# Kernel optimization log

Hardware: AMD Instinct MI355X
Metric: run time of the kernel (lower is better)

## Reference

```python
import jax, jax.numpy as jnp
import numpy as np

D = 512
N_WAY = 64
K_SHOT = 16
N_QUERY = 8192


def setup_inputs() -> dict:
    key = jax.random.key(0)
    k1, k2, k3, k4 = jax.random.split(key, 4)
    support = jax.random.normal(k1, (N_WAY * K_SHOT, D), dtype=jnp.float32)
    query = jax.random.normal(k2, (N_QUERY, D), dtype=jnp.float32)
    # nn.Linear(input_dim, input_dim) params (kaiming-uniform-ish scale)
    bound = 1.0 / np.sqrt(D)
    W = jax.random.uniform(k3, (D, D), minval=-bound, maxval=bound, dtype=jnp.float32)
    b = jax.random.uniform(k4, (D,), minval=-bound, maxval=bound, dtype=jnp.float32)
    return {"support": support, "query": query, "W": W, "b": b,
            "n_way": N_WAY, "k_shot": K_SHOT}


def reference(support, query, W, b, n_way, k_shot):
    # shared linear projection: x @ W^T + b (torch nn.Linear convention)
    support_emb = support @ W.T + b            # [n_way*k_shot, d]
    query_emb = query @ W.T + b                # [n_q, d]
    # class prototypes: mean over the k_shot axis
    prototypes = support_emb.reshape(n_way, k_shot, -1).mean(axis=1)  # [n_way, d]
    # pairwise squared euclidean distances (broadcast sub/square/sum,
    # same math as the torch euclidean_dist)
    diff = query_emb[:, None, :] - prototypes[None, :, :]  # [n_q, n_way, d]
    dists = jnp.sum(diff * diff, axis=-1)                  # [n_q, n_way]
    return dists
```

## Files before the change

### kernel.cpp

```cpp
#include <hip/hip_runtime.h>
#include <hip/hip_bf16.h>

#define D 512
#define NWAY 64
#define KSHOT 16
#define NQ 8192

typedef __bf16 bf16_t;
typedef __bf16 bf16x8_t __attribute__((ext_vector_type(8)));
typedef __bf16 bf16x4_t __attribute__((ext_vector_type(4)));
typedef float  f32x4    __attribute__((ext_vector_type(4)));

typedef __attribute__((address_space(1))) const void gv_t;
typedef __attribute__((address_space(3))) void lv_t;
__device__ __forceinline__ void ld16(const void* g, void* l) {
    __builtin_amdgcn_global_load_lds((gv_t*)g, (lv_t*)l, 16, 0, 0);
}


__global__ __launch_bounds__(256) void k_prep1(
    const float* __restrict__ sup, const float* __restrict__ W,
    const float* __restrict__ bias, float* __restrict__ Pg,
    bf16_t* __restrict__ Bsw)
{
    const int b = blockIdx.x, t = threadIdx.x;

    if (b < 256) {
        const int c = b >> 2, jq = b & 3;
        __shared__ __align__(16) float cm[D];
        {
            const int d = t * 2;
            float sx = 0.f, sy = 0.f;
#pragma unroll
            for (int j = 0; j < KSHOT; ++j) {
                float2 v = *(const float2*)(sup + (size_t)(c * KSHOT + j) * D + d);
                sx += v.x; sy += v.y;
            }
            cm[d] = sx * (1.0f / KSHOT); cm[d + 1] = sy * (1.0f / KSHOT);
        }
        __syncthreads();
        const int j = jq * 128 + (t >> 1);
        const int half = t & 1;
        const f32x4* wr = (const f32x4*)(W + (size_t)j * D + half * 256);
        const f32x4* cr = (const f32x4*)(cm + half * 256);
        float s = 0.f;
#pragma unroll 8
        for (int i = 0; i < 64; ++i) {
            f32x4 a = cr[i], wv = wr[i];
            s += a[0]*wv[0] + a[1]*wv[1] + a[2]*wv[2] + a[3]*wv[3];
        }
        s += __shfl_xor(s, 1);
        if (!half) Pg[(size_t)c * D + j] = s + bias[j];
        return;
    }

    {
        const int n = (b - 256) * 4 + (t >> 6);
        const int sl = t & 63;
        const f32x4* wp = (const f32x4*)(W + (size_t)n * D + sl * 8);
        f32x4 v0 = wp[0], v1 = wp[1];
        bf16x8_t hv = { (bf16_t)v0[0], (bf16_t)v0[1], (bf16_t)v0[2], (bf16_t)v0[3],
                        (bf16_t)v1[0], (bf16_t)v1[1], (bf16_t)v1[2], (bf16_t)v1[3] };
        const int ck = sl >> 3, s = sl & 7;
        *(bf16x8_t*)(Bsw + (size_t)ck * 36864 + n * 64 + ((s ^ (n & 7)) * 8)) = hv;
    }
}

__global__ __launch_bounds__(256) void k_prep2(
    const float* __restrict__ Pg, const float* __restrict__ W,
    const float* __restrict__ bias, bf16_t* __restrict__ Bsw,
    float* __restrict__ ph)
{
    __shared__ __align__(16) float Pl[D];
    __shared__ float sG[2][128];
    __shared__ float red[4];

    const int c = blockIdx.x >> 2, kc = blockIdx.x & 3;
    const int t = threadIdx.x;
    const int kl = t & 127, jh = t >> 7;
    const int k = kc * 128 + kl;

    ((float2*)Pl)[t] = ((const float2*)(Pg + (size_t)c * D))[t];
    __syncthreads();

    float g = 0.f;
    const float* wcol = W + (size_t)jh * 256 * D + k;
#pragma unroll 8
    for (int j = 0; j < 256; ++j)
        g += Pl[jh * 256 + j] * wcol[(size_t)j * D];
    sG[jh][kl] = g;

    if (kc == 0) {
        float v1 = Pl[t], v2 = Pl[t + 256];
        float pp = v1 * v1 - 2.0f * bias[t] * v1 + v2 * v2 - 2.0f * bias[t + 256] * v2;
#pragma unroll
        for (int off = 32; off; off >>= 1) pp += __shfl_xor(pp, off);
        if ((t & 63) == 0) red[t >> 6] = pp;
    }
    __syncthreads();

    if (jh == 0) {
        const float gt = sG[0][kl] + sG[1][kl];
        const int n = 512 + c;
        const int ck = k >> 6, s = (k >> 3) & 7, e = k & 7;
        Bsw[(size_t)ck * 36864 + n * 64 + ((s ^ (c & 7)) * 8) + e] = (bf16_t)gt;
    }
    if (kc == 0 && t == 0) ph[c] = red[0] + red[1] + red[2] + red[3];
}

__global__ __launch_bounds__(512, 2) void k_main(
    const float* __restrict__ query, const bf16_t* __restrict__ Bsw,
    const float* __restrict__ bias, const float* __restrict__ ph,
    float* __restrict__ out)
{
    __shared__ bf16_t Bb[2][36864];
    __shared__ bf16_t Ab[2][2048];
    __shared__ float qln[4][32];
    __shared__ float phs[NWAY];
    __shared__ float bs[576];

    const int t = threadIdx.x, bm = blockIdx.x;
    bs[t] = bias[t];
    if (t < NWAY) { bs[512 + t] = 0.f; phs[t] = ph[t]; }

    const int l = t & 63, w = t >> 6;
    const int wm = w & 1, wn = w >> 1;
    const int r15 = l & 15, quad = l >> 4;

    const int xt0 = ((quad ^ (r15 & 7)) * 8);
    const int xt1 = (((4 + quad) ^ (r15 & 7)) * 8);
    const int aoff = (wm * 16 + r15) * 64;
    const int boff = (wn * 144 + r15) * 64;
    const int wb = w * 4608 + l * 8;

    const int am = t >> 4;
    const int ac4 = t & 15;
    const int a_lds = am * 64 + (((ac4 >> 1) ^ (am & 7)) * 8) + (ac4 & 1) * 4;
    const float* aqp = query + (size_t)(bm * 32 + am) * D + ac4 * 4;

    bf16x4_t areg[8];
#pragma unroll
    for (int ck = 0; ck < 8; ++ck) {
        f32x4 v = *(const f32x4*)(aqp + ck * 64);
        areg[ck] = (bf16x4_t){ (bf16_t)v[0], (bf16_t)v[1], (bf16_t)v[2], (bf16_t)v[3] };
    }

    f32x4 acc[9];
#pragma unroll
    for (int i = 0; i < 9; ++i) acc[i] = (f32x4){0.f, 0.f, 0.f, 0.f};

    {
#pragma unroll
        for (int i = 0; i < 9; ++i)
            ld16(Bsw + wb + i * 512, &Bb[0][wb + i * 512]);
        *(bf16x4_t*)(&Ab[0][a_lds]) = areg[0];
    }
    __syncthreads();

#pragma unroll
    for (int ck = 0; ck < 8; ++ck) {
        const int cur = ck & 1;
        if (ck < 7) {
            const int nxt = cur ^ 1;
            const size_t sb = (size_t)(ck + 1) * 36864;
#pragma unroll
            for (int i = 0; i < 9; ++i)
                ld16(Bsw + sb + wb + i * 512, &Bb[nxt][wb + i * 512]);
            *(bf16x4_t*)(&Ab[nxt][a_lds]) = areg[ck + 1];
        }

        bf16x8_t a0 = *(const bf16x8_t*)(&Ab[cur][aoff + xt0]);
        bf16x8_t a1 = *(const bf16x8_t*)(&Ab[cur][aoff + xt1]);
#pragma unroll
        for (int tt = 0; tt < 9; ++tt) {
            bf16x8_t b0 = *(const bf16x8_t*)(&Bb[cur][boff + tt * 1024 + xt0]);
            bf16x8_t b1 = *(const bf16x8_t*)(&Bb[cur][boff + tt * 1024 + xt1]);
            acc[tt] = __builtin_amdgcn_mfma_f32_16x16x32_bf16(a0, b0, acc[tt], 0, 0, 0);
            acc[tt] = __builtin_amdgcn_mfma_f32_16x16x32_bf16(a1, b1, acc[tt], 0, 0, 0);
        }

        if (ck < 7) __syncthreads();
    }

    float qp[4] = {0.f, 0.f, 0.f, 0.f};
#pragma unroll
    for (int tt = 0; tt < 9; ++tt) {
        const int colbase = wn * 144 + tt * 16;
        const float m = (colbase < 512) ? 1.f : 0.f;
        const float bv = bs[colbase + r15];
#pragma unroll
        for (int reg = 0; reg < 4; ++reg) {
            float v = acc[tt][reg] + bv;
            qp[reg] += m * v * v;
        }
    }
#pragma unroll
    for (int reg = 0; reg < 4; ++reg) {
        float s = qp[reg];
        s += __shfl_xor(s, 1); s += __shfl_xor(s, 2);
        s += __shfl_xor(s, 4); s += __shfl_xor(s, 8);
        if (r15 == 0) qln[wn][wm * 16 + quad * 4 + reg] = s;
    }
    __syncthreads();

    if (wn == 3) {
#pragma unroll
        for (int reg = 0; reg < 4; ++reg) {
            const int row_local = quad * 4 + reg;
            const float qt = qln[0][wm * 16 + row_local] + qln[1][wm * 16 + row_local] +
                             qln[2][wm * 16 + row_local] + qln[3][wm * 16 + row_local];
            const int rowg = bm * 32 + wm * 16 + row_local;
#pragma unroll
            for (int tg = 0; tg < 4; ++tg) {
                const int c = tg * 16 + r15;
                out[(size_t)rowg * NWAY + c] = qt + phs[c] - 2.0f * acc[5 + tg][reg];
            }
        }
    }
}

extern "C" void kernel_launch(void* const* d_in, const int* in_sizes, int n_in,
                              void* d_out, int out_size, void* d_ws, size_t ws_size,
                              hipStream_t stream)
{
    const float* support = (const float*)d_in[0];
    const float* query   = (const float*)d_in[1];
    const float* W       = (const float*)d_in[2];
    const float* bias    = (const float*)d_in[3];
    float* out = (float*)d_out;

    char* ws = (char*)d_ws;
    bf16_t* Bsw = (bf16_t*)ws;
    float*  ph  = (float*)(ws + 589824);
    float*  Pg  = (float*)(ws + 589824 + 256);

    k_prep1<<<384, 256, 0, stream>>>(support, W, bias, Pg, Bsw);
    k_prep2<<<256, 256, 0, stream>>>(Pg, W, bias, Bsw, ph);
    k_main<<<256, 512, 0, stream>>>(query, Bsw, bias, ph, out);
}
```

Baseline: 110.6 us.

## Drop prototype-folded GEMM columns and compute query-prototype dot in epilogue

```diff
diff --git a/kernel.cpp b/kernel.cpp
--- a/kernel.cpp
+++ b/kernel.cpp
@@ -18,10 +18,10 @@
 }
 
 
-__global__ __launch_bounds__(256) void k_prep1(
+__global__ __launch_bounds__(256) void k_prep(
     const float* __restrict__ sup, const float* __restrict__ W,
-    const float* __restrict__ bias, float* __restrict__ Pg,
-    bf16_t* __restrict__ Bsw)
+    const float* __restrict__ bias, bf16_t* __restrict__ Bsw,
+    bf16_t* __restrict__ Psw)
 {
     const int b = blockIdx.x, t = threadIdx.x;
 
@@ -50,7 +50,12 @@
             s += a[0]*wv[0] + a[1]*wv[1] + a[2]*wv[2] + a[3]*wv[3];
         }
         s += __shfl_xor(s, 1);
-        if (!half) Pg[(size_t)c * D + j] = s + bias[j];
+        if (!half) {
+            const float v = s + bias[j];
+            const int sP = j >> 3;
+            const int pos = (sP & ~7) | ((sP & 7) ^ (c & 7));
+            Psw[c * 512 + pos * 8 + (j & 7)] = (bf16_t)v;
+        }
         return;
     }
 
@@ -62,66 +67,23 @@
         bf16x8_t hv = { (bf16_t)v0[0], (bf16_t)v0[1], (bf16_t)v0[2], (bf16_t)v0[3],
                         (bf16_t)v1[0], (bf16_t)v1[1], (bf16_t)v1[2], (bf16_t)v1[3] };
         const int ck = sl >> 3, s = sl & 7;
-        *(bf16x8_t*)(Bsw + (size_t)ck * 36864 + n * 64 + ((s ^ (n & 7)) * 8)) = hv;
-    }
-}
-
-__global__ __launch_bounds__(256) void k_prep2(
-    const float* __restrict__ Pg, const float* __restrict__ W,
-    const float* __restrict__ bias, bf16_t* __restrict__ Bsw,
-    float* __restrict__ ph)
-{
-    __shared__ __align__(16) float Pl[D];
-    __shared__ float sG[2][128];
-    __shared__ float red[4];
-
-    const int c = blockIdx.x >> 2, kc = blockIdx.x & 3;
-    const int t = threadIdx.x;
-    const int kl = t & 127, jh = t >> 7;
-    const int k = kc * 128 + kl;
-
-    ((float2*)Pl)[t] = ((const float2*)(Pg + (size_t)c * D))[t];
-    __syncthreads();
-
-    float g = 0.f;
-    const float* wcol = W + (size_t)jh * 256 * D + k;
-#pragma unroll 8
-    for (int j = 0; j < 256; ++j)
-        g += Pl[jh * 256 + j] * wcol[(size_t)j * D];
-    sG[jh][kl] = g;
-
-    if (kc == 0) {
-        float v1 = Pl[t], v2 = Pl[t + 256];
-        float pp = v1 * v1 - 2.0f * bias[t] * v1 + v2 * v2 - 2.0f * bias[t + 256] * v2;
-#pragma unroll
-        for (int off = 32; off; off >>= 1) pp += __shfl_xor(pp, off);
-        if ((t & 63) == 0) red[t >> 6] = pp;
-    }
-    __syncthreads();
-
-    if (jh == 0) {
-        const float gt = sG[0][kl] + sG[1][kl];
-        const int n = 512 + c;
-        const int ck = k >> 6, s = (k >> 3) & 7, e = k & 7;
-        Bsw[(size_t)ck * 36864 + n * 64 + ((s ^ (c & 7)) * 8) + e] = (bf16_t)gt;
-    }
-    if (kc == 0 && t == 0) ph[c] = red[0] + red[1] + red[2] + red[3];
+        *(bf16x8_t*)(Bsw + (size_t)ck * 32768 + n * 64 + ((s ^ (n & 7)) * 8)) = hv;
+    }
 }
 
 __global__ __launch_bounds__(512, 2) void k_main(
     const float* __restrict__ query, const bf16_t* __restrict__ Bsw,
-    const float* __restrict__ bias, const float* __restrict__ ph,
+    const bf16_t* __restrict__ Psw, const float* __restrict__ bias,
     float* __restrict__ out)
 {
-    __shared__ bf16_t Bb[2][36864];
-    __shared__ bf16_t Ab[2][2048];
+    __shared__ __align__(16) bf16_t Bb[2][32768];
+    __shared__ __align__(16) bf16_t Ab[2][2048];
     __shared__ float qln[4][32];
     __shared__ float phs[NWAY];
-    __shared__ float bs[576];
+    __shared__ float bs[512];
 
     const int t = threadIdx.x, bm = blockIdx.x;
     bs[t] = bias[t];
-    if (t < NWAY) { bs[512 + t] = 0.f; phs[t] = ph[t]; }
 
     const int l = t & 63, w = t >> 6;
     const int wm = w & 1, wn = w >> 1;
@@ -130,8 +92,7 @@
     const int xt0 = ((quad ^ (r15 & 7)) * 8);
     const int xt1 = (((4 + quad) ^ (r15 & 7)) * 8);
     const int aoff = (wm * 16 + r15) * 64;
-    const int boff = (wn * 144 + r15) * 64;
-    const int wb = w * 4608 + l * 8;
+    const int boff = (wn * 128 + r15) * 64;
 
     const int am = t >> 4;
     const int ac4 = t & 15;
@@ -145,14 +106,16 @@
         areg[ck] = (bf16x4_t){ (bf16_t)v[0], (bf16_t)v[1], (bf16_t)v[2], (bf16_t)v[3] };
     }
 
-    f32x4 acc[9];
-#pragma unroll
-    for (int i = 0; i < 9; ++i) acc[i] = (f32x4){0.f, 0.f, 0.f, 0.f};
+    f32x4 acc[8];
+#pragma unroll
+    for (int i = 0; i < 8; ++i) acc[i] = (f32x4){0.f, 0.f, 0.f, 0.f};
 
     {
 #pragma unroll
-        for (int i = 0; i < 9; ++i)
-            ld16(Bsw + wb + i * 512, &Bb[0][wb + i * 512]);
+        for (int i = 0; i < 8; ++i) {
+            const int off = t * 8 + i * 4096;
+            ld16(Bsw + off, &Bb[0][off]);
+        }
         *(bf16x4_t*)(&Ab[0][a_lds]) = areg[0];
     }
     __syncthreads();
@@ -162,17 +125,25 @@
         const int cur = ck & 1;
         if (ck < 7) {
             const int nxt = cur ^ 1;
-            const size_t sb = (size_t)(ck + 1) * 36864;
-#pragma unroll
-            for (int i = 0; i < 9; ++i)
-                ld16(Bsw + sb + wb + i * 512, &Bb[nxt][wb + i * 512]);
+            const size_t sb = (size_t)(ck + 1) * 32768;
+#pragma unroll
+            for (int i = 0; i < 8; ++i) {
+                const int off = t * 8 + i * 4096;
+                ld16(Bsw + sb + off, &Bb[nxt][off]);
+            }
             *(bf16x4_t*)(&Ab[nxt][a_lds]) = areg[ck + 1];
+        } else {
+#pragma unroll
+            for (int i = 0; i < 8; ++i) {
+                const int off = t * 8 + i * 4096;
+                ld16(Psw + off, &Bb[0][off]);
+            }
         }
 
         bf16x8_t a0 = *(const bf16x8_t*)(&Ab[cur][aoff + xt0]);
         bf16x8_t a1 = *(const bf16x8_t*)(&Ab[cur][aoff + xt1]);
 #pragma unroll
-        for (int tt = 0; tt < 9; ++tt) {
+        for (int tt = 0; tt < 8; ++tt) {
             bf16x8_t b0 = *(const bf16x8_t*)(&Bb[cur][boff + tt * 1024 + xt0]);
             bf16x8_t b1 = *(const bf16x8_t*)(&Bb[cur][boff + tt * 1024 + xt1]);
             acc[tt] = __builtin_amdgcn_mfma_f32_16x16x32_bf16(a0, b0, acc[tt], 0, 0, 0);
@@ -181,17 +152,22 @@
 
         if (ck < 7) __syncthreads();
     }
-
+    __syncthreads();
+
+    bf16_t* Ex = &Bb[1][0];
     float qp[4] = {0.f, 0.f, 0.f, 0.f};
 #pragma unroll
-    for (int tt = 0; tt < 9; ++tt) {
-        const int colbase = wn * 144 + tt * 16;
-        const float m = (colbase < 512) ? 1.f : 0.f;
-        const float bv = bs[colbase + r15];
+    for (int tt = 0; tt < 8; ++tt) {
+        const int k = wn * 128 + tt * 16 + r15;
+        const int s = k >> 3, klo = k & 7;
+        const float bv = bs[k];
 #pragma unroll
         for (int reg = 0; reg < 4; ++reg) {
-            float v = acc[tt][reg] + bv;
-            qp[reg] += m * v * v;
+            const int row = wm * 16 + quad * 4 + reg;
+            const float v = acc[tt][reg] + bv;
+            qp[reg] += v * v;
+            const int pos = (s & ~7) | ((s & 7) ^ (row & 7));
+            Ex[row * 512 + pos * 8 + klo] = (bf16_t)v;
         }
     }
 #pragma unroll
@@ -201,21 +177,55 @@
         s += __shfl_xor(s, 4); s += __shfl_xor(s, 8);
         if (r15 == 0) qln[wn][wm * 16 + quad * 4 + reg] = s;
     }
-    __syncthreads();
-
-    if (wn == 3) {
-#pragma unroll
-        for (int reg = 0; reg < 4; ++reg) {
-            const int row_local = quad * 4 + reg;
-            const float qt = qln[0][wm * 16 + row_local] + qln[1][wm * 16 + row_local] +
-                             qln[2][wm * 16 + row_local] + qln[3][wm * 16 + row_local];
-            const int rowg = bm * 32 + wm * 16 + row_local;
-#pragma unroll
-            for (int tg = 0; tg < 4; ++tg) {
-                const int c = tg * 16 + r15;
-                out[(size_t)rowg * NWAY + c] = qt + phs[c] - 2.0f * acc[5 + tg][reg];
-            }
-        }
+
+    if (t < NWAY) {
+        const bf16_t* pr = &Bb[0][t * 512];
+        float s2 = 0.f;
+#pragma unroll
+        for (int i = 0; i < 64; ++i) {
+            bf16x8_t v = *(const bf16x8_t*)(pr + i * 8);
+#pragma unroll
+            for (int e = 0; e < 8; ++e) { float f = (float)v[e]; s2 += f * f; }
+        }
+        phs[t] = s2;
+    }
+    __syncthreads();
+
+    f32x4 cacc[4];
+#pragma unroll
+    for (int ct = 0; ct < 4; ++ct) cacc[ct] = (f32x4){0.f, 0.f, 0.f, 0.f};
+    const bf16_t* Pl = &Bb[0][0];
+#pragma unroll
+    for (int kk = 0; kk < 4; ++kk) {
+        const int s = wn * 16 + kk * 4 + quad;
+        const int pos = (s & ~7) | ((s & 7) ^ (r15 & 7));
+        bf16x8_t af = *(const bf16x8_t*)(Ex + (wm * 16 + r15) * 512 + pos * 8);
+#pragma unroll
+        for (int ct = 0; ct < 4; ++ct) {
+            bf16x8_t bf = *(const bf16x8_t*)(Pl + (ct * 16 + r15) * 512 + pos * 8);
+            cacc[ct] = __builtin_amdgcn_mfma_f32_16x16x32_bf16(af, bf, cacc[ct], 0, 0, 0);
+        }
+    }
+
+    f32x4* ex = (f32x4*)&Bb[1][16384];
+#pragma unroll
+    for (int ct = 0; ct < 4; ++ct)
+        ex[((wm * 4 + ct) * 4 + wn) * 64 + l] = cacc[ct];
+    __syncthreads();
+
+    f32x4 cf = ex[((wm * 4 + wn) * 4 + 0) * 64 + l];
+#pragma unroll
+    for (int wnp = 1; wnp < 4; ++wnp)
+        cf = cf + ex[((wm * 4 + wn) * 4 + wnp) * 64 + l];
+
+#pragma unroll
+    for (int reg = 0; reg < 4; ++reg) {
+        const int row_local = wm * 16 + quad * 4 + reg;
+        const float qt = qln[0][row_local] + qln[1][row_local] +
+                         qln[2][row_local] + qln[3][row_local];
+        const int rowg = bm * 32 + row_local;
+        const int c = wn * 16 + r15;
+        out[(size_t)rowg * NWAY + c] = qt + phs[c] - 2.0f * cf[reg];
     }
 }
 
@@ -231,10 +241,8 @@
 
     char* ws = (char*)d_ws;
     bf16_t* Bsw = (bf16_t*)ws;
-    float*  ph  = (float*)(ws + 589824);
-    float*  Pg  = (float*)(ws + 589824 + 256);
-
-    k_prep1<<<384, 256, 0, stream>>>(support, W, bias, Pg, Bsw);
-    k_prep2<<<256, 256, 0, stream>>>(Pg, W, bias, Bsw, ph);
-    k_main<<<256, 512, 0, stream>>>(query, Bsw, bias, ph, out);
-}
+    bf16_t* Psw = (bf16_t*)(ws + 524288);
+
+    k_prep<<<384, 256, 0, stream>>>(support, W, bias, Bsw, Psw);
+    k_main<<<256, 512, 0, stream>>>(query, Bsw, Psw, bias, out);
+}
```

Measured after the change: 99.39 us, median of 2. 10.1% less time.
